# Performance work log

Measured on AMD Instinct MI355X. Metric: run time of the kernel, lower is better.

Reference implementation:

```python
import jax, jax.numpy as jnp
import numpy as np

EPS = 1e-14
RHO = 8.0


def _normalize(x):
    return x / jnp.linalg.norm(x, axis=-1, keepdims=True)


def setup_inputs() -> dict:
    key = jax.random.key(0)
    ks = jax.random.split(key, 12)
    B, D = 4096, 1024
    f = lambda k: _normalize(jax.random.normal(k, (B, D), dtype=jnp.float32))
    pos = lambda k: jax.random.uniform(k, (B, 1), dtype=jnp.float32, minval=0.1, maxval=1.0)
    return {
        "im_feat": f(ks[0]),
        "tt_feat": f(ks[1]),
        "rim_feat": f(ks[2]),
        "rtt_feat": f(ks[3]),
        "remote_u_im": pos(ks[4]),
        "remote_u_tt": pos(ks[5]),
        "loss1_im": pos(ks[6]),
        "loss1_tt": pos(ks[7]),
        "u_im": pos(ks[8]),
        "u_tt": pos(ks[9]),
        "logit_scale": 10.0 * jnp.ones((1,), dtype=jnp.float32),
        "offset": 0,
    }


def _pairwise_loss(rim, rtt, im, tt, logit_scale, offset):
    # features1 = remote, features2 = local (as in forward(): pairwise_loss(remote_features, features, ...))
    sim_image = rim @ tt.T                                  # [B1, B2]
    sim_text = rtt @ im.T                                   # [B1, B2]
    diag_sim = jnp.sum(rim * rtt, axis=-1, keepdims=True)   # [B1, 1]
    exp_im = jnp.exp((sim_image - diag_sim) * logit_scale)
    exp_tt = jnp.exp((sim_text - diag_sim) * logit_scale)
    B1, B2 = sim_image.shape
    # mask zeros the shifted diagonal: equivalent to subtracting the diagonal entry from the row sum
    cols = (jnp.arange(B1) + offset)[:, None]               # [B1, 1]
    rw_sum = B2 - 1 if B1 <= B2 else B2 * (B1 - 1) / B1
    loss_im = (jnp.sum(exp_im, axis=-1, keepdims=True)
               - jnp.take_along_axis(exp_im, cols, axis=1)) / rw_sum
    loss_tt = (jnp.sum(exp_tt, axis=-1, keepdims=True)
               - jnp.take_along_axis(exp_tt, cols, axis=1)) / rw_sum
    return loss_im, loss_tt


def reference(im_feat, tt_feat, rim_feat, rtt_feat, remote_u_im, remote_u_tt,
              loss1_im, loss1_tt, u_im, u_tt, logit_scale, offset):
    loss2_im, loss2_tt = _pairwise_loss(rim_feat, rtt_feat, im_feat, tt_feat, logit_scale, offset)
    pg1 = loss1_im / (u_im + EPS) + loss1_tt / (u_tt + EPS)
    pg2 = loss2_im / (remote_u_im + EPS) + loss2_tt / (remote_u_tt + EPS)
    loss = (jnp.mean(pg1) + jnp.mean(pg2)) / 2
    # multiply_tau branch
    ls = logit_scale[0]
    loss = loss / jax.lax.stop_gradient(ls)
    loss = loss + RHO / ls
    loss = loss + jnp.mean(jnp.log(u_im) + jnp.log(u_tt)) / 2 / ls
    return loss
```

## Files before the change

kernel.cpp:

```cpp
#include <hip/hip_runtime.h>
#include <hip/hip_bf16.h>

#define EPSF 1e-14f
#define RHOF 8.0f

typedef __attribute__((ext_vector_type(4))) float f32x4;
typedef __attribute__((ext_vector_type(8))) int   i32x8;
typedef __attribute__((ext_vector_type(2))) unsigned long long u64x2;

#define AS_GLOBAL __attribute__((address_space(1)))
#define AS_LDS    __attribute__((address_space(3)))


__global__ __launch_bounds__(256) void prep_fp8(
    const float* __restrict__ im,  const float* __restrict__ tt,
    const float* __restrict__ rim, const float* __restrict__ rtt,
    unsigned char* __restrict__ bIm,  unsigned char* __restrict__ bTt,
    unsigned char* __restrict__ bRim, unsigned char* __restrict__ bRtt,
    float* __restrict__ S_im, float* __restrict__ S_tt,
    float* __restrict__ diag, float* __restrict__ red,
    int D, int spm )
{
    __shared__ unsigned char L[8 * 1024];
    const int b = blockIdx.x;
    const int tid = threadIdx.x;
    const int nConv = 4 * spm;
    if (b < nConv) {
        int mIdx = b / spm;
        int slab = b - mIdx * spm;
        const float* src = (mIdx == 0) ? rim : (mIdx == 1) ? tt
                          : (mIdx == 2) ? rtt : im;
        unsigned char* dst = (mIdx == 0) ? bRim : (mIdx == 1) ? bTt
                            : (mIdx == 2) ? bRtt : bIm;
        const float* srow = src + (size_t)slab * 8 * D;
        const int n4 = (8 * D) >> 2;
        for (int idx = tid; idx < n4; idx += 256) {
            float4 v = *(const float4*)(srow + idx * 4);
            int pk = __builtin_amdgcn_cvt_pk_fp8_f32(v.x, v.y, 0, false);
            pk     = __builtin_amdgcn_cvt_pk_fp8_f32(v.z, v.w, pk, true);
            *(int*)&L[idx * 4] = pk;
        }
        __syncthreads();
        const int kTiles = D >> 7;
        const int rb = (slab * 8) >> 7;
        const int r0loc = (slab * 8) & 127;
        for (int g = tid; g < (D >> 1); g += 256) {
            int kb  = g >> 6;
            int rem = g & 63;
            int rl  = rem >> 3;
            int p   = rem & 7;
            int r   = slab * 8 + rl;
            int c   = p ^ (r & 7);
            const unsigned char* lb = &L[rl * D + kb * 128 + c * 16];
            u64x2 o = *(const u64x2*)lb;
            char* outp = (char*)dst
                       + ((size_t)(rb * kTiles + kb) * 1024
                          + (size_t)(r0loc + rl) * 8 + p) * 16;
            *(u64x2*)outp = o;
        }
    } else {
        int db = b - nConv;
        if (db == 0 && tid < 8) red[tid] = 0.f;
        if (tid < 4) { S_im[db * 4 + tid] = 0.f; S_tt[db * 4 + tid] = 0.f; }
        int row  = db * 4 + (tid >> 6);
        int lane = tid & 63;
        const float* a = rim + (size_t)row * D;
        const float* c = rtt + (size_t)row * D;
        float s = 0.f;
        for (int k = lane * 4; k < D; k += 256) {
            float4 av = *(const float4*)(a + k);
            float4 cv = *(const float4*)(c + k);
            s += av.x * cv.x + av.y * cv.y + av.z * cv.z + av.w * cv.w;
        }
        #pragma unroll
        for (int m2 = 1; m2 < 64; m2 <<= 1) s += __shfl_xor(s, m2, 64);
        if (lane == 0) diag[row] = s;
    }
}

__global__ __launch_bounds__(512, 2) void gemm_expsum(
    const unsigned char* __restrict__ A0, const unsigned char* __restrict__ B0,
    float* __restrict__ S0,
    const unsigned char* __restrict__ A1, const unsigned char* __restrict__ B1,
    float* __restrict__ S1,
    const float* __restrict__ logit_scale, const int* __restrict__ offset,
    int Bn, int D)
{
    const int z = blockIdx.z;
    const unsigned char* A = z ? A1 : A0;
    const unsigned char* B = z ? B1 : B0;
    float* S = z ? S1 : S0;

    __shared__ unsigned char As[2][32768];
    __shared__ unsigned char Bs[2][32768];

    const int tid  = threadIdx.x;
    const int wave = tid >> 6;
    const int lane = tid & 63;
    const int lo   = lane & 15;
    const int qd   = lane >> 4;
    const int wm   = wave >> 2;
    const int wn   = wave & 3;
    const int offA = ((2 * qd) ^ (lo & 7)) * 16;

    const int nx  = gridDim.x;
    const int nwg = nx * gridDim.y;
    int wg = blockIdx.y * nx + blockIdx.x;
    int swz = ((nwg & 7) == 0) ? ((wg & 7) * (nwg >> 3) + (wg >> 3)) : wg;
    const int by = swz / nx;
    const int bx = swz - by * nx;

    const int kTiles = D >> 7;
    const unsigned char* Atile = A + (size_t)(2 * by) * kTiles * 16384;
    const unsigned char* Btile = B + (size_t)(2 * bx) * kTiles * 16384;

    auto stage = [&](int buf, int kb) {
        #pragma unroll
        for (int h = 0; h < 2; ++h) {
            const size_t tbase = (size_t)(h * kTiles + kb) * 16384;
            #pragma unroll
            for (int i = 0; i < 2; ++i) {
                const int u    = (i * 512 + tid) * 16;
                const int loff = h * 16384 + i * 8192 + wave * 1024;
                __builtin_amdgcn_global_load_lds(
                    (const AS_GLOBAL unsigned int*)(Atile + tbase + u),
                    (AS_LDS unsigned int*)&As[buf][loff], 16, 0, 0);
                __builtin_amdgcn_global_load_lds(
                    (const AS_GLOBAL unsigned int*)(Btile + tbase + u),
                    (AS_LDS unsigned int*)&Bs[buf][loff], 16, 0, 0);
            }
        }
    };

    f32x4 acc[8][4];
    #pragma unroll
    for (int i = 0; i < 8; ++i)
        #pragma unroll
        for (int j = 0; j < 4; ++j)
            acc[i][j] = (f32x4){0.f, 0.f, 0.f, 0.f};

    const int aOff0 = wm * 16384 + lo * 128 + offA;
    const int bOff0 = (wn >> 1) * 16384 + ((wn & 1) * 64 + lo) * 128 + offA;

    stage(0, 0);
    __syncthreads();

    for (int kb = 0; kb < kTiles; ++kb) {
        const int cur = kb & 1;
        if (kb + 1 < kTiles)
            stage(1 - cur, kb + 1);
        i32x8 bq[4];
        #pragma unroll
        for (int tj = 0; tj < 4; ++tj) {
            const int ba = bOff0 + tj * 2048;
            union { int4 h[2]; i32x8 v; } u;
            u.h[0] = *(const int4*)&Bs[cur][ba];
            u.h[1] = *(const int4*)&Bs[cur][ba ^ 16];
            bq[tj] = u.v;
        }
        #pragma unroll
        for (int ti = 0; ti < 8; ++ti) {
            const int aa = aOff0 + ti * 2048;
            union { int4 h[2]; i32x8 v; } u;
            u.h[0] = *(const int4*)&As[cur][aa];
            u.h[1] = *(const int4*)&As[cur][aa ^ 16];
            i32x8 af = u.v;
            __builtin_amdgcn_s_setprio(1);
            #pragma unroll
            for (int tj = 0; tj < 4; ++tj)
                acc[ti][tj] = __builtin_amdgcn_mfma_scale_f32_16x16x128_f8f6f4(
                    af, bq[tj], acc[ti][tj],
                    0, 0,
                    0, 127,
                    0, 127);
            __builtin_amdgcn_s_setprio(0);
        }
        __syncthreads();
    }

    const float ls = logit_scale[0];
    const int offs = offset[0];
    const int rowBase = by * 256 + wm * 128;
    const int colBase = bx * 256 + wn * 64;
    #pragma unroll
    for (int ti = 0; ti < 8; ++ti) {
        #pragma unroll
        for (int r = 0; r < 4; ++r) {
            int gi = rowBase + 16 * ti + 4 * qd + r;
            float rs = 0.f;
            #pragma unroll
            for (int tj = 0; tj < 4; ++tj) {
                int gj = colBase + 16 * tj + lo;
                float e = __expf(ls * acc[ti][tj][r]);
                if (gj == gi + offs) e = 0.f;
                rs += e;
            }
            #pragma unroll
            for (int m = 1; m < 16; m <<= 1) rs += __shfl_xor(rs, m, 64);
            if (lo == 0) atomicAdd(&S[gi], rs);
        }
    }
}

__global__ __launch_bounds__(256) void final_kernel(
    const float* __restrict__ S_im, const float* __restrict__ S_tt,
    const float* __restrict__ diag,
    const float* __restrict__ ru_im, const float* __restrict__ ru_tt,
    const float* __restrict__ l1_im, const float* __restrict__ l1_tt,
    const float* __restrict__ u_im,  const float* __restrict__ u_tt,
    const float* __restrict__ logit_scale, float* __restrict__ red,
    float* __restrict__ out, int Bn)
{
    const float ls = logit_scale[0];
    const float inv_rw = 1.0f / (float)(Bn - 1);
    const int gid = blockIdx.x * 256 + threadIdx.x;
    float pg = 0.f, lg = 0.f;
    for (int i = gid; i < Bn; i += 8 * 256) {
        float p1 = l1_im[i] / (u_im[i] + EPSF) + l1_tt[i] / (u_tt[i] + EPSF);
        float dd = expf(-ls * diag[i]);
        float p2 = dd * S_im[i] * inv_rw / (ru_im[i] + EPSF)
                 + dd * S_tt[i] * inv_rw / (ru_tt[i] + EPSF);
        pg += p1 + p2;
        lg += logf(u_im[i]) + logf(u_tt[i]);
    }
    __shared__ float sp[256], sl[256];
    sp[threadIdx.x] = pg; sl[threadIdx.x] = lg;
    __syncthreads();
    for (int s = 128; s > 0; s >>= 1) {
        if (threadIdx.x < s) { sp[threadIdx.x] += sp[threadIdx.x + s];
                               sl[threadIdx.x] += sl[threadIdx.x + s]; }
        __syncthreads();
    }
    if (threadIdx.x == 0) {
        atomicAdd(&red[0], sp[0]);
        atomicAdd(&red[1], sl[0]);
        __threadfence();
        int t = atomicAdd((int*)&red[2], 1);
        if (t == gridDim.x - 1) {
            float pgSum = atomicAdd(&red[0], 0.f);
            float lgSum = atomicAdd(&red[1], 0.f);
            float loss = ((pgSum / (float)Bn) * 0.5f) / ls
                       + RHOF / ls
                       + (lgSum / (float)Bn) * 0.5f / ls;
            out[0] = loss;
        }
    }
}

extern "C" void kernel_launch(void* const* d_in, const int* in_sizes, int n_in,
                              void* d_out, int out_size, void* d_ws, size_t ws_size,
                              hipStream_t stream) {
    const float* im    = (const float*)d_in[0];
    const float* tt    = (const float*)d_in[1];
    const float* rim   = (const float*)d_in[2];
    const float* rtt   = (const float*)d_in[3];
    const float* ru_im = (const float*)d_in[4];
    const float* ru_tt = (const float*)d_in[5];
    const float* l1_im = (const float*)d_in[6];
    const float* l1_tt = (const float*)d_in[7];
    const float* u_im  = (const float*)d_in[8];
    const float* u_tt  = (const float*)d_in[9];
    const float* lsc   = (const float*)d_in[10];
    const int*   offs  = (const int*)d_in[11];

    const int Bn = in_sizes[4];
    const int D  = in_sizes[0] / Bn;
    const int spm = Bn / 8;

    char* base = (char*)d_ws;
    float* S_im = (float*)base;
    float* S_tt = S_im + Bn;
    float* diag = S_tt + Bn;
    float* red  = diag + Bn;
    const size_t headBytes = (((size_t)(3 * Bn + 8) * sizeof(float)) + 255) & ~(size_t)255;
    const size_t matBytes  = (size_t)Bn * D;
    unsigned char* buf0 = (unsigned char*)(base + headBytes);
    unsigned char* bRim = buf0;
    unsigned char* bTt  = buf0 + matBytes;
    unsigned char* bRtt = buf0 + 2 * matBytes;
    unsigned char* bIm  = buf0 + 3 * matBytes;

    prep_fp8<<<4 * spm + Bn / 4, 256, 0, stream>>>(
        im, tt, rim, rtt, bIm, bTt, bRim, bRtt, S_im, S_tt, diag, red, D, spm);

    dim3 ggrid(Bn / 256, Bn / 256, 2);
    gemm_expsum<<<ggrid, 512, 0, stream>>>(bRim, bTt, S_im, bRtt, bIm, S_tt,
                                           lsc, offs, Bn, D);

    final_kernel<<<8, 256, 0, stream>>>(S_im, S_tt, diag, ru_im, ru_tt,
                                        l1_im, l1_tt, u_im, u_tt, lsc,
                                        red, (float*)d_out, Bn);
}
```

Baseline: 181.9 us.

## Assign per-wave tile ownership for async loads and add phased barrier scheduling in GEMM

Reorganizes the global-to-LDS staging so each wave loads a contiguous 8 KB slice of one operand tile, instead of every thread contributing to every tile. The main loop is split into four phases of two A-fragments each, with explicit s_barrier calls around the MFMA bursts to keep waves in lockstep. The end-of-iteration __syncthreads is replaced by an explicit vmcnt wait plus barrier. The aim is to overlap loads with MFMAs and cut issue contention, at the cost of many more barriers per k-tile, which may stall waves.

```diff
diff --git a/kernel.cpp b/kernel.cpp
--- a/kernel.cpp
+++ b/kernel.cpp
@@ -114,22 +114,23 @@
     const unsigned char* Atile = A + (size_t)(2 * by) * kTiles * 16384;
     const unsigned char* Btile = B + (size_t)(2 * bx) * kTiles * 16384;
 
-    auto stage = [&](int buf, int kb) {
-        #pragma unroll
-        for (int h = 0; h < 2; ++h) {
-            const size_t tbase = (size_t)(h * kTiles + kb) * 16384;
-            #pragma unroll
-            for (int i = 0; i < 2; ++i) {
-                const int u    = (i * 512 + tid) * 16;
-                const int loff = h * 16384 + i * 8192 + wave * 1024;
-                __builtin_amdgcn_global_load_lds(
-                    (const AS_GLOBAL unsigned int*)(Atile + tbase + u),
-                    (AS_LDS unsigned int*)&As[buf][loff], 16, 0, 0);
-                __builtin_amdgcn_global_load_lds(
-                    (const AS_GLOBAL unsigned int*)(Btile + tbase + u),
-                    (AS_LDS unsigned int*)&Bs[buf][loff], 16, 0, 0);
-            }
-        }
+    const int half = wave >> 1;
+    const int part = wave & 1;
+    const unsigned char* ownerG =
+        (half < 2) ? Atile + (size_t)half * kTiles * 16384
+                   : Btile + (size_t)(half - 2) * kTiles * 16384;
+    const unsigned char* ownerGL = ownerG + part * 8192 + lane * 16;
+    const int ownerLoff = (half & 1) * 16384 + part * 8192;
+    const bool ownerIsA = (half < 2);
+
+    auto stageOwner = [&](int buf, int kb) {
+        const unsigned char* g = ownerGL + (size_t)kb * 16384;
+        unsigned char* l = (ownerIsA ? &As[buf][0] : &Bs[buf][0]) + ownerLoff;
+        #pragma unroll
+        for (int q = 0; q < 8; ++q)
+            __builtin_amdgcn_global_load_lds(
+                (const AS_GLOBAL unsigned int*)(g + q * 1024),
+                (AS_LDS unsigned int*)(l + q * 1024), 16, 0, 0);
     };
 
     f32x4 acc[8][4];
@@ -142,13 +143,15 @@
     const int aOff0 = wm * 16384 + lo * 128 + offA;
     const int bOff0 = (wn >> 1) * 16384 + ((wn & 1) * 64 + lo) * 128 + offA;
 
-    stage(0, 0);
-    __syncthreads();
+    stageOwner(0, 0);
+    asm volatile("s_waitcnt vmcnt(0)" ::: "memory");
+    __builtin_amdgcn_s_barrier();
 
     for (int kb = 0; kb < kTiles; ++kb) {
         const int cur = kb & 1;
         if (kb + 1 < kTiles)
-            stage(1 - cur, kb + 1);
+            stageOwner(1 - cur, kb + 1);
+
         i32x8 bq[4];
         #pragma unroll
         for (int tj = 0; tj < 4; ++tj) {
@@ -158,24 +161,39 @@
             u.h[1] = *(const int4*)&Bs[cur][ba ^ 16];
             bq[tj] = u.v;
         }
-        #pragma unroll
-        for (int ti = 0; ti < 8; ++ti) {
-            const int aa = aOff0 + ti * 2048;
-            union { int4 h[2]; i32x8 v; } u;
-            u.h[0] = *(const int4*)&As[cur][aa];
-            u.h[1] = *(const int4*)&As[cur][aa ^ 16];
-            i32x8 af = u.v;
+
+        #pragma unroll
+        for (int ph = 0; ph < 4; ++ph) {
+            const int ti0 = 2 * ph;
+            union { int4 h[2]; i32x8 v; } ua0, ua1;
+            {
+                const int aa0 = aOff0 + ti0 * 2048;
+                ua0.h[0] = *(const int4*)&As[cur][aa0];
+                ua0.h[1] = *(const int4*)&As[cur][aa0 ^ 16];
+                const int aa1 = aOff0 + (ti0 + 1) * 2048;
+                ua1.h[0] = *(const int4*)&As[cur][aa1];
+                ua1.h[1] = *(const int4*)&As[cur][aa1 ^ 16];
+            }
+            __builtin_amdgcn_s_barrier();
             __builtin_amdgcn_s_setprio(1);
             #pragma unroll
             for (int tj = 0; tj < 4; ++tj)
-                acc[ti][tj] = __builtin_amdgcn_mfma_scale_f32_16x16x128_f8f6f4(
-                    af, bq[tj], acc[ti][tj],
-                    0, 0,
-                    0, 127,
-                    0, 127);
+                acc[ti0][tj] = __builtin_amdgcn_mfma_scale_f32_16x16x128_f8f6f4(
+                    ua0.v, bq[tj], acc[ti0][tj],
+                    0, 0, 0, 127, 0, 127);
+            #pragma unroll
+            for (int tj = 0; tj < 4; ++tj)
+                acc[ti0 + 1][tj] = __builtin_amdgcn_mfma_scale_f32_16x16x128_f8f6f4(
+                    ua1.v, bq[tj], acc[ti0 + 1][tj],
+                    0, 0, 0, 127, 0, 127);
             __builtin_amdgcn_s_setprio(0);
-        }
-        __syncthreads();
+            __builtin_amdgcn_s_barrier();
+        }
+
+        if (kb + 1 < kTiles) {
+            asm volatile("s_waitcnt vmcnt(0)" ::: "memory");
+            __builtin_amdgcn_s_barrier();
+        }
     }
 
     const float ls = logit_scale[0];
```

Result: faster. 178.0 us (-2.1%).
